# Optimization experiments

Hardware: AMD Instinct MI355X
Metric: run time of the kernel (lower is better)

The kernel has to match this reference:

```python
import jax, jax.numpy as jnp
import numpy as np

B, T, C = 2, 2048, 2048
NH, NKV = 16, 4
HD = C // NH  # 128


def _rope(x, cos, sin):
    d = x.shape[-1] // 2
    x1, x2 = x[..., :d], x[..., d:]
    return jnp.concatenate([x1 * cos + x2 * sin, -x1 * sin + x2 * cos], axis=-1)


def _rmsnorm(x):
    eps = jnp.finfo(x.dtype).eps
    return x * jax.lax.rsqrt(jnp.mean(jnp.square(x), axis=-1, keepdims=True) + eps)


def setup_inputs() -> dict:
    key = jax.random.key(0)
    ks = jax.random.split(key, 7)
    s = 0.02
    return {
        "x": jax.random.normal(ks[0], (B, T, C), jnp.float32),
        "cos": jax.random.normal(ks[1], (1, T, 1, HD // 2), jnp.float32),
        "sin": jax.random.normal(ks[2], (1, T, 1, HD // 2), jnp.float32),
        "wq": jax.random.normal(ks[3], (C, NH * HD), jnp.float32) * s,
        "wk": jax.random.normal(ks[4], (C, NKV * HD), jnp.float32) * s,
        "wv": jax.random.normal(ks[5], (C, NKV * HD), jnp.float32) * s,
        "wo": jax.random.normal(ks[6], (C, C), jnp.float32) * s,
    }


def reference(x, cos, sin, wq, wk, wv, wo):
    q = (x @ wq).reshape(B, T, NH, HD)
    k = (x @ wk).reshape(B, T, NKV, HD)
    v = (x @ wv).reshape(B, T, NKV, HD)
    q = _rmsnorm(_rope(q, cos, sin))
    k = _rmsnorm(_rope(k, cos, sin))
    # [B, H, T, D]
    q = q.transpose(0, 2, 1, 3)
    k = k.transpose(0, 2, 1, 3)
    v = v.transpose(0, 2, 1, 3)
    rep = NH // NKV
    k = jnp.repeat(k, rep, axis=1)
    v = jnp.repeat(v, rep, axis=1)
    scale = 1.0 / jnp.sqrt(jnp.float32(HD))
    scores = jnp.einsum("bhqd,bhkd->bhqk", q, k) * scale
    causal = jnp.tril(jnp.ones((T, T), bool))
    scores = jnp.where(causal, scores, jnp.finfo(scores.dtype).min)
    attn = jax.nn.softmax(scores, axis=-1)
    y = jnp.einsum("bhqk,bhkd->bhqd", attn, v)
    y = y.transpose(0, 2, 1, 3).reshape(B, T, C)
    return y @ wo
```

## Files before the change

### kernel.cpp

```cpp
#include <hip/hip_runtime.h>
#include <hip/hip_bf16.h>
#include <cstdint>

typedef unsigned short u16;
typedef __bf16 bf16x8 __attribute__((ext_vector_type(8)));
typedef float f32x4 __attribute__((ext_vector_type(4)));
typedef unsigned short u16x4 __attribute__((ext_vector_type(4)));
typedef unsigned uint2v __attribute__((ext_vector_type(2)));

#define B_ 2
#define T_ 2048
#define C_ 2048
#define NH_ 16
#define NKV_ 4
#define HD_ 128
#define K2_ 0.12752004650581538f

__device__ __forceinline__ u16 f2bf(float f) {
    unsigned u = __builtin_bit_cast(unsigned, f);
    unsigned r = u + 0x7FFFu + ((u >> 16) & 1u);
    return (u16)(r >> 16);
}

__device__ __forceinline__ unsigned cvtpk(float a, float b) {
    unsigned r;
    asm("v_cvt_pk_bf16_f32 %0, %1, %2" : "=v"(r) : "v"(a), "v"(b));
    return r;
}

__device__ __forceinline__ void gl16(const void* g, void* l) {
    auto gp = reinterpret_cast<const __attribute__((address_space(1))) unsigned*>(
        reinterpret_cast<uintptr_t>(g));
    auto lp = reinterpret_cast<__attribute__((address_space(3))) unsigned*>(
        reinterpret_cast<uintptr_t>(l));
    __builtin_amdgcn_global_load_lds(gp, lp, 16, 0, 0);
}

__global__ void transpose_conv(const float* __restrict__ in, u16* __restrict__ out, int N) {
    __shared__ float tile[32][33];
    int n0 = blockIdx.x * 32, k0 = blockIdx.y * 32;
    int tx = threadIdx.x, ty = threadIdx.y;
#pragma unroll
    for (int i = 0; i < 4; ++i)
        tile[ty * 4 + i][tx] = in[(size_t)(k0 + ty * 4 + i) * N + n0 + tx];
    __syncthreads();
#pragma unroll
    for (int i = 0; i < 4; ++i)
        out[(size_t)(n0 + ty * 4 + i) * 2048 + k0 + tx] = f2bf(tile[tx][ty * 4 + i]);
}

__global__ void convert4(const float4* __restrict__ in, u16* __restrict__ out) {
    int i = blockIdx.x * 256 + threadIdx.x;
    float4 v = in[i];
    u16x4 o;
    o[0] = f2bf(v.x); o[1] = f2bf(v.y); o[2] = f2bf(v.z); o[3] = f2bf(v.w);
    ((u16x4*)out)[i] = o;
}

__global__ __launch_bounds__(256, 2) void gemm_bf16(const u16* __restrict__ A,
                                                    const u16* __restrict__ BT,
                                                    float* __restrict__ C, int N, int K) {
    __shared__ __align__(16) u16 As[2][128 * 64];
    __shared__ __align__(16) u16 Bs[2][128 * 64];
    int nwg = gridDim.x * gridDim.y;
    int bid = blockIdx.y * gridDim.x + blockIdx.x;
    int nb = (bid & 7) * (nwg >> 3) + (bid >> 3);
    int bx = nb % gridDim.x, by = nb / gridDim.x;

    int t = threadIdx.x;
    int w = t >> 6, l = t & 63;
    int wr = w >> 1, wc = w & 1;
    int lg = l >> 4, lr = l & 15;
    int m0 = by * 128, n0 = bx * 128;
    f32x4 acc[4][4] = {};

    size_t goff[4];
#pragma unroll
    for (int i = 0; i < 4; ++i) {
        int g = t + i * 256;
        goff[i] = (size_t)(g >> 3) * K * 2 + (size_t)(((g & 7) ^ ((g >> 3) & 7)) * 16);
    }
    const char* Ab = (const char*)A + (size_t)m0 * K * 2;
    const char* Bb = (const char*)BT + (size_t)n0 * K * 2;

    auto stage = [&](int kt, int buf) {
        char* Ad = (char*)As[buf] + t * 16;
        char* Bd = (char*)Bs[buf] + t * 16;
#pragma unroll
        for (int i = 0; i < 4; ++i) {
            gl16(Ab + (size_t)kt * 2 + goff[i], Ad + i * 4096);
            gl16(Bb + (size_t)kt * 2 + goff[i], Bd + i * 4096);
        }
    };

    stage(0, 0);
    int nk = K >> 6;
    for (int ki = 0; ki < nk; ++ki) {
        asm volatile("s_waitcnt vmcnt(0)" ::: "memory");
        __builtin_amdgcn_s_barrier();
        __builtin_amdgcn_sched_barrier(0);
        int cur = ki & 1;
        if (ki + 1 < nk) stage((ki + 1) * 64, cur ^ 1);
#pragma unroll
        for (int kk = 0; kk < 2; ++kk) {
            bf16x8 af[4], bfr[4];
#pragma unroll
            for (int m = 0; m < 4; ++m)
                af[m] = *(const bf16x8*)&As[cur][(wr * 64 + m * 16 + lr) * 64 +
                                                (((kk * 4 + lg) ^ (lr & 7)) * 8)];
#pragma unroll
            for (int n = 0; n < 4; ++n)
                bfr[n] = *(const bf16x8*)&Bs[cur][(wc * 64 + n * 16 + lr) * 64 +
                                                 (((kk * 4 + lg) ^ (lr & 7)) * 8)];
#pragma unroll
            for (int m = 0; m < 4; ++m)
#pragma unroll
                for (int n = 0; n < 4; ++n)
                    acc[m][n] = __builtin_amdgcn_mfma_f32_16x16x32_bf16(af[m], bfr[n], acc[m][n], 0, 0, 0);
        }
    }
#pragma unroll
    for (int m = 0; m < 4; ++m) {
        int row = m0 + wr * 64 + m * 16 + lg * 4;
#pragma unroll
        for (int n = 0; n < 4; ++n) {
            int col = n0 + wc * 64 + n * 16 + lr;
            float* Cp = C + (size_t)row * N + col;
#pragma unroll
            for (int r = 0; r < 4; ++r)
                Cp[(size_t)r * N] = acc[m][n][r];
        }
    }
}

__global__ void rope_rms(const float* __restrict__ qkv, const float* __restrict__ cs,
                         const float* __restrict__ sn, u16* __restrict__ qh,
                         u16* __restrict__ kh) {
    int task = blockIdx.x * 4 + (threadIdx.x >> 6);
    int l = threadIdx.x & 63;
    const float* in;
    u16* out;
    int tpos;
    float post = 1.0f;
    if (task < 65536) {
        int row = task >> 4, h = task & 15;
        in = qkv + (size_t)row * 3072 + h * 128;
        int b = row >> 11; tpos = row & 2047;
        out = qh + ((size_t)(b * NH_ + h) * T_ + tpos) * HD_;
        post = K2_;
    } else {
        int t2 = task - 65536;
        int row = t2 >> 2, h = t2 & 3;
        in = qkv + (size_t)row * 3072 + 2048 + h * 128;
        int b = row >> 11; tpos = row & 2047;
        out = kh + ((size_t)(b * NKV_ + h) * T_ + tpos) * HD_;
    }
    float x1 = in[l], x2 = in[l + 64];
    float c = cs[tpos * 64 + l], s = sn[tpos * 64 + l];
    float o1 = x1 * c + x2 * s;
    float o2 = -x1 * s + x2 * c;
    float ss = o1 * o1 + o2 * o2;
#pragma unroll
    for (int m = 1; m < 64; m <<= 1) ss += __shfl_xor(ss, m);
    float r = rsqrtf(ss * (1.0f / 128.0f) + 1.1920929e-07f) * post;
    out[l] = f2bf(o1 * r);
    out[l + 64] = f2bf(o2 * r);
}

__global__ void transpose_v(const float* __restrict__ qkv, u16* __restrict__ vt) {
    __shared__ float tile[32][33];
    int t0 = blockIdx.x * 32;
    int d0 = blockIdx.y * 32;
    int bk = blockIdx.z;
    int b = bk >> 2, kvh = bk & 3;
    int tx = threadIdx.x, ty = threadIdx.y;
#pragma unroll
    for (int i = 0; i < 4; ++i)
        tile[ty * 4 + i][tx] =
            qkv[(size_t)(b * 2048 + t0 + ty * 4 + i) * 3072 + 2560 + kvh * 128 + d0 + tx];
    __syncthreads();
#pragma unroll
    for (int i = 0; i < 4; ++i)
        vt[((size_t)bk * 128 + d0 + ty * 4 + i) * 2048 + t0 + tx] = f2bf(tile[tx][ty * 4 + i]);
}

__global__ __launch_bounds__(256, 2) void attn(const u16* __restrict__ Q,
                                               const u16* __restrict__ Kk,
                                               const u16* __restrict__ V,
                                               u16* __restrict__ Y) {
    extern __shared__ __align__(16) u16 sm[];
    u16* Ks = sm;
    u16* Vs = sm + 16384;
    u16* Pb = sm + 32768;

    int bid = blockIdx.x;
    int xcd = bid & 7;
    int b = xcd >> 2, kvh = xcd & 3;
    int q = bid >> 3;
    int j = (q < 32) ? (63 - q) : (q - 32);
    int NN = (j >> 1) + 1;
    int t = threadIdx.x;
    int w = t >> 6, l = t & 63;
    int lg = l >> 4, lr = l & 15;
    int h = kvh * 4 + w;
    int qw = j * 32;

    const u16* Qp = Q + (size_t)(b * NH_ + h) * T_ * HD_;
    const u16* Kp = Kk + (size_t)(b * NKV_ + kvh) * T_ * HD_;
    const u16* Vp = V + (size_t)(b * NKV_ + kvh) * HD_ * T_;
    u16* Yp = Y + (size_t)(b * T_) * 2048 + h * HD_;
    u16* Pw = Pb + w * 1024;

    size_t koff[4], voff[4];
#pragma unroll
    for (int i = 0; i < 4; ++i) {
        int g = t + i * 256;
        koff[i] = (size_t)(g >> 4) * 256 + (size_t)(((g & 15) ^ ((g >> 4) & 15)) * 16);
        voff[i] = (size_t)(g >> 3) * (T_ * 2) + (size_t)(((g & 7) ^ ((g >> 3) & 7)) * 16);
    }
    auto stage = [&](int kv0, int buf) {
        const char* Kb = (const char*)Kp + (size_t)kv0 * 256;
        const char* Vb = (const char*)Vp + (size_t)kv0 * 2;
        char* Kd = (char*)Ks + buf * 16384 + t * 16;
        char* Vd = (char*)Vs + buf * 16384 + t * 16;
#pragma unroll
        for (int i = 0; i < 4; ++i) {
            gl16(Kb + koff[i], Kd + i * 4096);
            gl16(Vb + voff[i], Vd + i * 4096);
        }
    };

    bf16x8 aq[2][4];
#pragma unroll
    for (int qf = 0; qf < 2; ++qf)
#pragma unroll
        for (int ch = 0; ch < 4; ++ch)
            aq[qf][ch] = *(const bf16x8*)(Qp + (size_t)(qw + qf * 16 + lr) * HD_ + ch * 32 + lg * 8);

    f32x4 acc[2][8] = {};
    float m2[2] = {-1e30f, -1e30f};
    float lp_[2] = {0.0f, 0.0f};

    stage(0, 0);

    for (int gi = 0; gi < NN; ++gi) {
        asm volatile("s_waitcnt vmcnt(0)" ::: "memory");
        __builtin_amdgcn_s_barrier();
        __builtin_amdgcn_sched_barrier(0);
        int cur = gi & 1;
        if (gi + 1 < NN) stage((gi + 1) * 64, cur ^ 1);
        int kv0 = gi * 64;
        int kbase = cur * 8192;

        f32x4 sc[2][4] = {};
        __builtin_amdgcn_s_setprio(1);
#pragma unroll
        for (int ch = 0; ch < 4; ++ch)
#pragma unroll
            for (int kf = 0; kf < 4; ++kf) {
                bf16x8 bk = *(const bf16x8*)&Ks[kbase + (kf * 16 + lr) * 128 + (((ch * 4 + lg) ^ lr) * 8)];
                sc[0][kf] = __builtin_amdgcn_mfma_f32_16x16x32_bf16(bk, aq[0][ch], sc[0][kf], 0, 0, 0);
                sc[1][kf] = __builtin_amdgcn_mfma_f32_16x16x32_bf16(bk, aq[1][ch], sc[1][kf], 0, 0, 0);
            }
        __builtin_amdgcn_s_setprio(0);

        if (kv0 + 63 > qw) {
#pragma unroll
            for (int qf = 0; qf < 2; ++qf) {
                int qrow = qw + qf * 16 + lr;
#pragma unroll
                for (int kf = 0; kf < 4; ++kf)
#pragma unroll
                    for (int r = 0; r < 4; ++r) {
                        int key = kv0 + kf * 16 + 4 * lg + r;
                        if (key > qrow) sc[qf][kf][r] = -1e38f;
                    }
            }
        }
        float mx[2];
#pragma unroll
        for (int qf = 0; qf < 2; ++qf) {
            float m = sc[qf][0][0];
#pragma unroll
            for (int kf = 0; kf < 4; ++kf)
#pragma unroll
                for (int r = 0; r < 4; ++r) m = fmaxf(m, sc[qf][kf][r]);
            m = fmaxf(m, __shfl_xor(m, 16));
            m = fmaxf(m, __shfl_xor(m, 32));
            mx[qf] = m;
        }
        bool upd = (mx[0] > m2[0] + 8.0f) || (mx[1] > m2[1] + 8.0f);
        if (__any(upd)) {
#pragma unroll
            for (int qf = 0; qf < 2; ++qf) {
                float mn = fmaxf(m2[qf], mx[qf]);
                float rs = exp2f(m2[qf] - mn);
                m2[qf] = mn;
                lp_[qf] *= rs;
                float rs4[4];
#pragma unroll
                for (int r = 0; r < 4; ++r) rs4[r] = __shfl(rs, 4 * lg + r, 16);
#pragma unroll
                for (int oc = 0; oc < 8; ++oc)
#pragma unroll
                    for (int r = 0; r < 4; ++r) acc[qf][oc][r] *= rs4[r];
            }
        }
        bf16x8 ap[2][2];
#pragma unroll
        for (int kk = 0; kk < 2; ++kk) {
#pragma unroll
            for (int qf = 0; qf < 2; ++qf) {
                float ps = 0.0f;
#pragma unroll
                for (int kfl = 0; kfl < 2; ++kfl) {
                    int kf = kk * 2 + kfl;
                    float p0 = exp2f(sc[qf][kf][0] - m2[qf]);
                    float p1 = exp2f(sc[qf][kf][1] - m2[qf]);
                    float p2 = exp2f(sc[qf][kf][2] - m2[qf]);
                    float p3 = exp2f(sc[qf][kf][3] - m2[qf]);
                    ps += (p0 + p1) + (p2 + p3);
                    uint2v pk;
                    pk[0] = cvtpk(p0, p1);
                    pk[1] = cvtpk(p2, p3);
                    int g = 2 * kfl + (lg >> 1);
                    *(uint2v*)&Pw[(qf * 16 + lr) * 32 + ((g ^ (lr & 3)) * 8) + (lg & 1) * 4] = pk;
                }
                lp_[qf] += ps;
            }
#pragma unroll
            for (int qf = 0; qf < 2; ++qf)
                ap[qf][kk] = *(const bf16x8*)&Pw[(qf * 16 + lr) * 32 + ((lg ^ (lr & 3)) * 8)];
        }
        __builtin_amdgcn_s_setprio(1);
#pragma unroll
        for (int oc = 0; oc < 8; ++oc)
#pragma unroll
            for (int kk = 0; kk < 2; ++kk) {
                bf16x8 bv = *(const bf16x8*)&Vs[kbase + (oc * 16 + lr) * 64 +
                                                (((kk * 4 + lg) ^ (lr & 7)) * 8)];
                acc[0][oc] = __builtin_amdgcn_mfma_f32_16x16x32_bf16(ap[0][kk], bv, acc[0][oc], 0, 0, 0);
                acc[1][oc] = __builtin_amdgcn_mfma_f32_16x16x32_bf16(ap[1][kk], bv, acc[1][oc], 0, 0, 0);
            }
        __builtin_amdgcn_s_setprio(0);
    }
#pragma unroll
    for (int qf = 0; qf < 2; ++qf) {
        float lt = lp_[qf];
        lt += __shfl_xor(lt, 16);
        lt += __shfl_xor(lt, 32);
        float inv = 1.0f / lt;
        float inv4[4];
#pragma unroll
        for (int r = 0; r < 4; ++r) inv4[r] = __shfl(inv, 4 * lg + r, 16);
#pragma unroll
        for (int oc = 0; oc < 8; ++oc)
#pragma unroll
            for (int r = 0; r < 4; ++r)
                Yp[(size_t)(qw + qf * 16 + 4 * lg + r) * 2048 + oc * 16 + lr] =
                    f2bf(acc[qf][oc][r] * inv4[r]);
    }
}

extern "C" void kernel_launch(void* const* d_in, const int* in_sizes, int n_in,
                              void* d_out, int out_size, void* d_ws, size_t ws_size,
                              hipStream_t stream) {
    const float* x    = (const float*)d_in[0];
    const float* cosT = (const float*)d_in[1];
    const float* sinT = (const float*)d_in[2];
    const float* wq   = (const float*)d_in[3];
    const float* wk   = (const float*)d_in[4];
    const float* wv   = (const float*)d_in[5];
    const float* wo   = (const float*)d_in[6];
    float* out = (float*)d_out;

    char* ws = (char*)d_ws;
    u16*   wqkvT = (u16*)(ws);
    u16*   woT   = (u16*)(ws + 12582912);
    u16*   xb    = (u16*)(ws + 20971520);
    float* qkv   = (float*)(ws + 37748736);
    u16*   qh    = (u16*)(ws + 88080384);
    u16*   kh    = (u16*)(ws + 104857600);
    u16*   vt    = (u16*)(ws + 109051904);
    u16*   y     = xb;

    hipFuncSetAttribute(reinterpret_cast<const void*>(&attn),
                        hipFuncAttributeMaxDynamicSharedMemorySize, 73728);

    transpose_conv<<<dim3(64, 64), dim3(32, 8), 0, stream>>>(wq, wqkvT, 2048);
    transpose_conv<<<dim3(16, 64), dim3(32, 8), 0, stream>>>(wk, wqkvT + (size_t)2048 * 2048, 512);
    transpose_conv<<<dim3(16, 64), dim3(32, 8), 0, stream>>>(wv, wqkvT + (size_t)2560 * 2048, 512);
    transpose_conv<<<dim3(64, 64), dim3(32, 8), 0, stream>>>(wo, woT, 2048);
    convert4<<<8192, 256, 0, stream>>>((const float4*)x, xb);

    gemm_bf16<<<dim3(24, 32), 256, 0, stream>>>(xb, wqkvT, qkv, 3072, 2048);

    rope_rms<<<20480, 256, 0, stream>>>(qkv, cosT, sinT, qh, kh);
    transpose_v<<<dim3(64, 4, 8), dim3(32, 8), 0, stream>>>(qkv, vt);

    attn<<<512, 256, 73728, stream>>>(qh, kh, vt, y);

    gemm_bf16<<<dim3(16, 32), 256, 0, stream>>>(y, woT, out, 2048, 2048);
}
```

Measured before the change: 206.9 us.

## Pair causal query tiles per block and read V tiles directly into registers

Each attention block now handles two query tiles, j and 63-j, in one 33-step loop so every block does equal causal work, and the grid is halved to 256 blocks. V is re-laid out by transpose_v into contiguous 64-key tiles and loaded straight from global memory into registers instead of being staged in LDS, which cuts shared memory to 40 KB. The softmax row sum now comes from an MFMA against a ones vector rather than scalar adds and shuffles. The trade-offs: occupancy is reduced via launch_bounds(256,1) with only one block's worth of work per CU, and the direct global V loads may expose latency that LDS staging used to hide.

```diff
diff --git a/kernel.cpp b/kernel.cpp
--- a/kernel.cpp
+++ b/kernel.cpp
@@ -179,77 +179,121 @@
         tile[ty * 4 + i][tx] =
             qkv[(size_t)(b * 2048 + t0 + ty * 4 + i) * 3072 + 2560 + kvh * 128 + d0 + tx];
     __syncthreads();
-#pragma unroll
-    for (int i = 0; i < 4; ++i)
-        vt[((size_t)bk * 128 + d0 + ty * 4 + i) * 2048 + t0 + tx] = f2bf(tile[tx][ty * 4 + i]);
-}
-
-__global__ __launch_bounds__(256, 2) void attn(const u16* __restrict__ Q,
+    int tb = t0 >> 6;
+    int c0 = t0 & 32;
+#pragma unroll
+    for (int i = 0; i < 4; ++i) {
+        int d = d0 + ty * 4 + i;
+        vt[(((size_t)bk * 32 + tb) * 128 + d) * 64 + c0 + tx] = f2bf(tile[tx][ty * 4 + i]);
+    }
+}
+
+__global__ __launch_bounds__(256, 1) void attn(const u16* __restrict__ Q,
                                                const u16* __restrict__ Kk,
-                                               const u16* __restrict__ V,
+                                               const u16* __restrict__ Vt,
                                                u16* __restrict__ Y) {
     extern __shared__ __align__(16) u16 sm[];
     u16* Ks = sm;
-    u16* Vs = sm + 16384;
-    u16* Pb = sm + 32768;
+    u16* Pb = sm + 16384;
 
     int bid = blockIdx.x;
     int xcd = bid & 7;
     int b = xcd >> 2, kvh = xcd & 3;
-    int q = bid >> 3;
-    int j = (q < 32) ? (63 - q) : (q - 32);
-    int NN = (j >> 1) + 1;
+    int j = bid >> 3;
+    int NA = (j >> 1) + 1;
     int t = threadIdx.x;
     int w = t >> 6, l = t & 63;
     int lg = l >> 4, lr = l & 15;
     int h = kvh * 4 + w;
-    int qw = j * 32;
+    int qwA = j * 32, qwB = (63 - j) * 32;
 
     const u16* Qp = Q + (size_t)(b * NH_ + h) * T_ * HD_;
     const u16* Kp = Kk + (size_t)(b * NKV_ + kvh) * T_ * HD_;
-    const u16* Vp = V + (size_t)(b * NKV_ + kvh) * HD_ * T_;
+    const u16* Vb = Vt + (size_t)(b * NKV_ + kvh) * 32 * 8192;
     u16* Yp = Y + (size_t)(b * T_) * 2048 + h * HD_;
     u16* Pw = Pb + w * 1024;
 
-    size_t koff[4], voff[4];
+    size_t koff[4];
 #pragma unroll
     for (int i = 0; i < 4; ++i) {
         int g = t + i * 256;
         koff[i] = (size_t)(g >> 4) * 256 + (size_t)(((g & 15) ^ ((g >> 4) & 15)) * 16);
-        voff[i] = (size_t)(g >> 3) * (T_ * 2) + (size_t)(((g & 7) ^ ((g >> 3) & 7)) * 16);
-    }
-    auto stage = [&](int kv0, int buf) {
+    }
+    auto stageK = [&](int kv0, int buf) {
         const char* Kb = (const char*)Kp + (size_t)kv0 * 256;
-        const char* Vb = (const char*)Vp + (size_t)kv0 * 2;
         char* Kd = (char*)Ks + buf * 16384 + t * 16;
-        char* Vd = (char*)Vs + buf * 16384 + t * 16;
-#pragma unroll
-        for (int i = 0; i < 4; ++i) {
-            gl16(Kb + koff[i], Kd + i * 4096);
-            gl16(Vb + voff[i], Vd + i * 4096);
-        }
+#pragma unroll
+        for (int i = 0; i < 4; ++i) gl16(Kb + koff[i], Kd + i * 4096);
     };
 
     bf16x8 aq[2][4];
-#pragma unroll
-    for (int qf = 0; qf < 2; ++qf)
-#pragma unroll
-        for (int ch = 0; ch < 4; ++ch)
-            aq[qf][ch] = *(const bf16x8*)(Qp + (size_t)(qw + qf * 16 + lr) * HD_ + ch * 32 + lg * 8);
+    auto loadQ = [&](int qw2) {
+#pragma unroll
+        for (int qf = 0; qf < 2; ++qf)
+#pragma unroll
+            for (int ch = 0; ch < 4; ++ch)
+                aq[qf][ch] = *(const bf16x8*)(Qp + (size_t)(qw2 + qf * 16 + lr) * HD_ + ch * 32 + lg * 8);
+    };
+
+    bf16x8 ones;
+#pragma unroll
+    for (int i = 0; i < 8; ++i) ones[i] = __builtin_bit_cast(__bf16, (u16)0x3F80);
 
     f32x4 acc[2][8] = {};
+    f32x4 accl[2] = {};
     float m2[2] = {-1e30f, -1e30f};
-    float lp_[2] = {0.0f, 0.0f};
-
-    stage(0, 0);
-
-    for (int gi = 0; gi < NN; ++gi) {
+
+    auto epi = [&](int qw2) {
+#pragma unroll
+        for (int qf = 0; qf < 2; ++qf) {
+            float inv4[4];
+#pragma unroll
+            for (int r = 0; r < 4; ++r) inv4[r] = 1.0f / accl[qf][r];
+#pragma unroll
+            for (int oc = 0; oc < 8; ++oc)
+#pragma unroll
+                for (int r = 0; r < 4; ++r)
+                    Yp[(size_t)(qw2 + qf * 16 + 4 * lg + r) * 2048 + oc * 16 + lr] =
+                        f2bf(acc[qf][oc][r] * inv4[r]);
+        }
+    };
+
+    loadQ(qwA);
+    int qw = qwA;
+    stageK(0, 0);
+
+    for (int gi = 0; gi < 33; ++gi) {
         asm volatile("s_waitcnt vmcnt(0)" ::: "memory");
         __builtin_amdgcn_s_barrier();
         __builtin_amdgcn_sched_barrier(0);
         int cur = gi & 1;
-        if (gi + 1 < NN) stage((gi + 1) * 64, cur ^ 1);
-        int kv0 = gi * 64;
+        int kvT = (gi < NA) ? gi : gi - NA;
+        if (gi + 1 < 33) {
+            int gn = gi + 1;
+            stageK((gn < NA ? gn : gn - NA) * 64, cur ^ 1);
+        }
+        const u16* Vtile = Vb + (size_t)kvT * 8192;
+        bf16x8 vreg[16];
+#pragma unroll
+        for (int oc = 0; oc < 8; ++oc)
+#pragma unroll
+            for (int kk = 0; kk < 2; ++kk)
+                vreg[oc * 2 + kk] = *(const bf16x8*)&Vtile[(oc * 16 + lr) * 64 + kk * 32 + lg * 8];
+        __builtin_amdgcn_sched_barrier(0);
+
+        if (gi == NA) {
+            epi(qwA);
+#pragma unroll
+            for (int qf = 0; qf < 2; ++qf) {
+#pragma unroll
+                for (int oc = 0; oc < 8; ++oc) acc[qf][oc] = f32x4{0.f, 0.f, 0.f, 0.f};
+                accl[qf] = f32x4{0.f, 0.f, 0.f, 0.f};
+                m2[qf] = -1e30f;
+            }
+            loadQ(qwB);
+            qw = qwB;
+        }
+        int kv0 = kvT * 64;
         int kbase = cur * 8192;
 
         f32x4 sc[2][4] = {};
@@ -296,7 +340,6 @@
                 float mn = fmaxf(m2[qf], mx[qf]);
                 float rs = exp2f(m2[qf] - mn);
                 m2[qf] = mn;
-                lp_[qf] *= rs;
                 float rs4[4];
 #pragma unroll
                 for (int r = 0; r < 4; ++r) rs4[r] = __shfl(rs, 4 * lg + r, 16);
@@ -304,6 +347,8 @@
                 for (int oc = 0; oc < 8; ++oc)
 #pragma unroll
                     for (int r = 0; r < 4; ++r) acc[qf][oc][r] *= rs4[r];
+#pragma unroll
+                for (int r = 0; r < 4; ++r) accl[qf][r] *= rs4[r];
             }
         }
         bf16x8 ap[2][2];
@@ -311,7 +356,6 @@
         for (int kk = 0; kk < 2; ++kk) {
 #pragma unroll
             for (int qf = 0; qf < 2; ++qf) {
-                float ps = 0.0f;
 #pragma unroll
                 for (int kfl = 0; kfl < 2; ++kfl) {
                     int kf = kk * 2 + kfl;
@@ -319,14 +363,12 @@
                     float p1 = exp2f(sc[qf][kf][1] - m2[qf]);
                     float p2 = exp2f(sc[qf][kf][2] - m2[qf]);
                     float p3 = exp2f(sc[qf][kf][3] - m2[qf]);
-                    ps += (p0 + p1) + (p2 + p3);
                     uint2v pk;
                     pk[0] = cvtpk(p0, p1);
                     pk[1] = cvtpk(p2, p3);
                     int g = 2 * kfl + (lg >> 1);
                     *(uint2v*)&Pw[(qf * 16 + lr) * 32 + ((g ^ (lr & 3)) * 8) + (lg & 1) * 4] = pk;
                 }
-                lp_[qf] += ps;
             }
 #pragma unroll
             for (int qf = 0; qf < 2; ++qf)
@@ -334,32 +376,20 @@
         }
         __builtin_amdgcn_s_setprio(1);
 #pragma unroll
+        for (int qf = 0; qf < 2; ++qf)
+#pragma unroll
+            for (int kk = 0; kk < 2; ++kk)
+                accl[qf] = __builtin_amdgcn_mfma_f32_16x16x32_bf16(ap[qf][kk], ones, accl[qf], 0, 0, 0);
+#pragma unroll
         for (int oc = 0; oc < 8; ++oc)
 #pragma unroll
             for (int kk = 0; kk < 2; ++kk) {
-                bf16x8 bv = *(const bf16x8*)&Vs[kbase + (oc * 16 + lr) * 64 +
-                                                (((kk * 4 + lg) ^ (lr & 7)) * 8)];
-                acc[0][oc] = __builtin_amdgcn_mfma_f32_16x16x32_bf16(ap[0][kk], bv, acc[0][oc], 0, 0, 0);
-                acc[1][oc] = __builtin_amdgcn_mfma_f32_16x16x32_bf16(ap[1][kk], bv, acc[1][oc], 0, 0, 0);
+                acc[0][oc] = __builtin_amdgcn_mfma_f32_16x16x32_bf16(ap[0][kk], vreg[oc * 2 + kk], acc[0][oc], 0, 0, 0);
+                acc[1][oc] = __builtin_amdgcn_mfma_f32_16x16x32_bf16(ap[1][kk], vreg[oc * 2 + kk], acc[1][oc], 0, 0, 0);
             }
         __builtin_amdgcn_s_setprio(0);
     }
-#pragma unroll
-    for (int qf = 0; qf < 2; ++qf) {
-        float lt = lp_[qf];
-        lt += __shfl_xor(lt, 16);
-        lt += __shfl_xor(lt, 32);
-        float inv = 1.0f / lt;
-        float inv4[4];
-#pragma unroll
-        for (int r = 0; r < 4; ++r) inv4[r] = __shfl(inv, 4 * lg + r, 16);
-#pragma unroll
-        for (int oc = 0; oc < 8; ++oc)
-#pragma unroll
-            for (int r = 0; r < 4; ++r)
-                Yp[(size_t)(qw + qf * 16 + 4 * lg + r) * 2048 + oc * 16 + lr] =
-                    f2bf(acc[qf][oc][r] * inv4[r]);
-    }
+    epi(qwB);
 }
 
 extern "C" void kernel_launch(void* const* d_in, const int* in_sizes, int n_in,
@@ -385,7 +415,7 @@
     u16*   y     = xb;
 
     hipFuncSetAttribute(reinterpret_cast<const void*>(&attn),
-                        hipFuncAttributeMaxDynamicSharedMemorySize, 73728);
+                        hipFuncAttributeMaxDynamicSharedMemorySize, 40960);
 
     transpose_conv<<<dim3(64, 64), dim3(32, 8), 0, stream>>>(wq, wqkvT, 2048);
     transpose_conv<<<dim3(16, 64), dim3(32, 8), 0, stream>>>(wk, wqkvT + (size_t)2048 * 2048, 512);
@@ -398,7 +428,7 @@
     rope_rms<<<20480, 256, 0, stream>>>(qkv, cosT, sinT, qh, kh);
     transpose_v<<<dim3(64, 4, 8), dim3(32, 8), 0, stream>>>(qkv, vt);
 
-    attn<<<512, 256, 73728, stream>>>(qh, kh, vt, y);
+    attn<<<256, 256, 40960, stream>>>(qh, kh, vt, y);
 
     gemm_bf16<<<dim3(16, 32), 256, 0, stream>>>(y, woT, out, 2048, 2048);
 }
```

Measured after the change: 272.3 us. +31.6%, slower.
